# Performance work log

Hardware: AMD Instinct MI355X
Metric: run time of the kernel (lower is better)

Reference implementation:

```python
import jax, jax.numpy as jnp
import numpy as np

DIM, H, KV, HD = 2048, 32, 8, 64
NREP = H // KV
EPS = 1e-6
NEG = -1e30


def _rope(x, cos, sin):
    # x: [B,S,h,HD], cos/sin: [S,HD//2]
    xr, xi = x[..., 0::2], x[..., 1::2]
    c = cos[None, :, None, :]
    s = sin[None, :, None, :]
    out = jnp.stack([xr * c - xi * s, xr * s + xi * c], axis=-1)
    return out.reshape(x.shape)


def _rmsnorm(x, w):
    xf = x.astype(jnp.float32)
    inv = jax.lax.rsqrt(jnp.mean(xf * xf, axis=-1, keepdims=True) + EPS)
    return (xf * inv * w).astype(x.dtype)


def setup_inputs() -> dict:
    key = jax.random.key(0)
    ks = jax.random.split(key, 9)
    B, S = 1, 2048
    x = jax.random.normal(ks[0], (B, S, DIM), jnp.float32)
    cos = jax.random.uniform(ks[1], (S, HD // 2), jnp.float32)
    sin = jax.random.uniform(ks[2], (S, HD // 2), jnp.float32)
    sc = 1.0 / np.sqrt(DIM)
    wq = jax.random.normal(ks[3], (DIM, DIM), jnp.float32) * sc
    wk = jax.random.normal(ks[4], (KV * HD, DIM), jnp.float32) * sc
    wv = jax.random.normal(ks[5], (KV * HD, DIM), jnp.float32) * sc
    wo = jax.random.normal(ks[6], (DIM, DIM), jnp.float32) * sc
    wg = jax.random.normal(ks[7], (DIM, DIM), jnp.float32) * sc
    qn = jnp.ones((HD,), jnp.float32)
    kn = jnp.ones((HD,), jnp.float32)
    return {"x": x, "cos": cos, "sin": sin, "wq": wq, "wk": wk, "wv": wv,
            "wo": wo, "wg": wg, "qn": qn, "kn": kn}


def reference(x, cos, sin, wq, wk, wv, wo, wg, qn, kn):
    B, S, _ = x.shape
    q = (x @ wq.T).reshape(B, S, H, HD)
    k = (x @ wk.T).reshape(B, S, KV, HD)
    v = (x @ wv.T).reshape(B, S, KV, HD)
    q = _rope(q, cos, sin)
    k = _rope(k, cos, sin)
    q = _rmsnorm(q, qn)
    k = _rmsnorm(k, kn)
    # GQA without materializing repeat_kv: head h = g*NREP + r uses kv head g
    qg = q.reshape(B, S, KV, NREP, HD)
    scale = 1.0 / np.sqrt(HD)
    scores = jnp.einsum('bqgrd,bkgd->bgrqk', qg, k) * scale  # [B,KV,NREP,S,S]
    causal = jnp.tril(jnp.ones((S, S), bool))
    scores = jnp.where(causal, scores, NEG)
    attn = jax.nn.softmax(scores, axis=-1)
    o = jnp.einsum('bgrqk,bkgd->bqgrd', attn, v).reshape(B, S, DIM)
    o = o * jax.nn.sigmoid(x @ wg.T)
    return o @ wo.T
```

## Files before the change

### kernel.cpp

```cpp
#include <hip/hip_runtime.h>
#include <stdint.h>

typedef unsigned short u16;
typedef __bf16 bf16x8 __attribute__((ext_vector_type(8)));
typedef float f32x4 __attribute__((ext_vector_type(4)));

__device__ __forceinline__ float bf2f(u16 u) {
  union { unsigned int i; float f; } v; v.i = ((unsigned int)u) << 16; return v.f;
}
__device__ __forceinline__ u16 f2bf(float f) {
  union { float f; unsigned int i; } v; v.f = f;
  unsigned int r = v.i + 0x7fffu + ((v.i >> 16) & 1u);
  return (u16)(r >> 16);
}
__device__ __forceinline__ u16 f2bf_trunc(float f) {
  union { float f; unsigned int i; } v; v.f = f;
  return (u16)(v.i >> 16);
}
__device__ __forceinline__ void ld16(const void* g, void* l) {
  __builtin_amdgcn_global_load_lds(
      (const __attribute__((address_space(1))) unsigned int*)g,
      (__attribute__((address_space(3))) unsigned int*)l, 16, 0, 0);
}

__global__ __launch_bounds__(256) void k_cast(
    const float* __restrict__ s0, u16* __restrict__ d0,
    const float* __restrict__ s1, u16* __restrict__ d1,
    const float* __restrict__ s2, u16* __restrict__ d2,
    const float* __restrict__ s3, u16* __restrict__ d3,
    const float* __restrict__ s4, u16* __restrict__ d4,
    const float* __restrict__ s5, u16* __restrict__ d5)
{
  int b = blockIdx.x;
  const float* s; u16* d;
  if (b < 4096)       { s = s0; d = d0; }
  else if (b < 8192)  { s = s1; d = d1; b -= 4096; }
  else if (b < 9216)  { s = s2; d = d2; b -= 8192; }
  else if (b < 10240) { s = s3; d = d3; b -= 9216; }
  else if (b < 14336) { s = s4; d = d4; b -= 10240; }
  else                { s = s5; d = d5; b -= 14336; }
  const int i = (b * 256 + threadIdx.x) * 4;
  const float4 v = *(const float4*)(s + i);
  ushort4 o;
  o.x = f2bf(v.x); o.y = f2bf(v.y); o.z = f2bf(v.z); o.w = f2bf(v.w);
  *(ushort4*)(d + i) = o;
}

template <typename OT>
__device__ __forceinline__ void gemm_body(
    const u16* __restrict__ A, int lda,
    const u16* __restrict__ B, int ldb,
    OT* __restrict__ C, int ldc, int K,
    u16* As, u16* Bs)
{
  const int tid = threadIdx.x;
  const int wave = tid >> 6, lane = tid & 63;
  const int wrow = (wave >> 1) * 64, wcol = (wave & 1) * 64;
  const int fr = lane & 15, kg = lane >> 4;
  const int srl = lane >> 3;
  const int scg = (lane & 7) ^ srl;

  f32x4 acc[4][4];
  const f32x4 z = {0.f, 0.f, 0.f, 0.f};
  for (int i = 0; i < 4; i++) for (int j = 0; j < 4; j++) acc[i][j] = z;

  const u16* Ag = A + (size_t)(wave * 8 + srl) * lda + scg * 8;
  const u16* Bg = B + (size_t)(wave * 8 + srl) * ldb + scg * 8;
  u16* Asw = As + wave * 8 * 64;
  u16* Bsw = Bs + wave * 8 * 64;
  const int sxr = fr & 7;

  for (int k0 = 0; k0 < K; k0 += 64) {
    for (int i = 0; i < 4; i++) {
      ld16(Ag + k0 + (size_t)(i * 32) * lda, Asw + i * 32 * 64);
      ld16(Bg + k0 + (size_t)(i * 32) * ldb, Bsw + i * 32 * 64);
    }
    __syncthreads();
    bf16x8 af[4][2], bfr[4][2];
    for (int i = 0; i < 4; i++)
      for (int h = 0; h < 2; h++) {
        af[i][h]  = *(const bf16x8*)&As[(wrow + i * 16 + fr) * 64 + (((h * 4 + kg) ^ sxr)) * 8];
        bfr[i][h] = *(const bf16x8*)&Bs[(wcol + i * 16 + fr) * 64 + (((h * 4 + kg) ^ sxr)) * 8];
      }
    for (int h = 0; h < 2; h++)
      for (int mi = 0; mi < 4; mi++)
        for (int ni = 0; ni < 4; ni++)
          acc[mi][ni] = __builtin_amdgcn_mfma_f32_16x16x32_bf16(af[mi][h], bfr[ni][h], acc[mi][ni], 0, 0, 0);
    __syncthreads();
  }
  const int er = kg * 4, ec = fr;
  for (int mi = 0; mi < 4; mi++)
    for (int ni = 0; ni < 4; ni++)
      for (int r = 0; r < 4; r++) {
        const float v = acc[mi][ni][r];
        OT* p = C + (size_t)(wrow + mi * 16 + er + r) * ldc + wcol + ni * 16 + ec;
        if constexpr (sizeof(OT) == 2) *p = (OT)f2bf(v); else *p = (OT)v;
      }
}

__global__ __launch_bounds__(256) void k_gemm_qkvg(
    const u16* __restrict__ x, const u16* __restrict__ wq, const u16* __restrict__ wk,
    const u16* __restrict__ wv, const u16* __restrict__ wg, u16* __restrict__ out)
{
  __shared__ __align__(16) u16 As[128 * 64];
  __shared__ __align__(16) u16 Bs[128 * 64];
  const int m0 = blockIdx.x * 128;
  const int c0 = blockIdx.y * 128;
  const u16* B; int br;
  if (c0 < 2048)      { B = wq; br = c0; }
  else if (c0 < 2560) { B = wk; br = c0 - 2048; }
  else if (c0 < 3072) { B = wv; br = c0 - 2560; }
  else                { B = wg; br = c0 - 3072; }
  gemm_body<u16>(x + (size_t)m0 * 2048, 2048, B + (size_t)br * 2048, 2048,
                 out + (size_t)m0 * 5120 + c0, 5120, 2048, As, Bs);
}

__global__ __launch_bounds__(256) void k_gemm_out(
    const u16* __restrict__ a, const u16* __restrict__ wo, float* __restrict__ out)
{
  __shared__ __align__(16) u16 As[128 * 64];
  __shared__ __align__(16) u16 Bs[128 * 64];
  const int m0 = blockIdx.x * 128;
  const int c0 = blockIdx.y * 128;
  gemm_body<float>(a + (size_t)m0 * 2048, 2048, wo + (size_t)c0 * 2048, 2048,
                   out + (size_t)m0 * 2048 + c0, 2048, 2048, As, Bs);
}

__global__ __launch_bounds__(256) void k_prep(
    u16* __restrict__ qkvg, const float* __restrict__ cosp, const float* __restrict__ sinp,
    const float* __restrict__ qn, const float* __restrict__ kn, u16* __restrict__ vt)
{
  __shared__ u16 Ls[64 * 72];
  if (blockIdx.x < 10240) {
    const int wid = (blockIdx.x * 256 + threadIdx.x) >> 6;
    const int lane = threadIdx.x & 63;
    const int s = wid / 20, hp = wid - s * 20;
    const int h = hp * 2 + (lane >> 5);
    const int j = lane & 31;
    u16* base; const float* wn;
    if (h < 32) { base = qkvg + (size_t)s * 5120 + h * 64;                wn = qn; }
    else        { base = qkvg + (size_t)s * 5120 + 2048 + (h - 32) * 64; wn = kn; }
    const unsigned int u = *(const unsigned int*)(base + 2 * j);
    const float xr = bf2f((u16)(u & 0xffffu)), xi = bf2f((u16)(u >> 16));
    const float c = cosp[s * 32 + j], sn = sinp[s * 32 + j];
    const float o0 = xr * c - xi * sn;
    const float o1 = xr * sn + xi * c;
    float ss = o0 * o0 + o1 * o1;
    for (int m = 1; m <= 16; m <<= 1) ss += __shfl_xor(ss, m, 64);
    const float inv = rsqrtf(ss * (1.0f / 64.0f) + 1e-6f);
    const u16 r0 = f2bf(o0 * inv * wn[2 * j]);
    const u16 r1 = f2bf(o1 * inv * wn[2 * j + 1]);
    *(unsigned int*)(base + 2 * j) = (unsigned int)r0 | ((unsigned int)r1 << 16);
  } else {
    const int bb = blockIdx.x - 10240;
    const int s0 = (bb & 31) * 64, g0 = (bb >> 5) * 64;
    const int tid = threadIdx.x;
    const int lr = tid >> 4, lc = (tid & 15) * 4;
    for (int p = 0; p < 4; p++) {
      const int r = p * 16 + lr;
      *(ushort4*)&Ls[r * 72 + lc] = *(const ushort4*)&qkvg[(size_t)(s0 + r) * 5120 + 2560 + g0 + lc];
    }
    __syncthreads();
    for (int p = 0; p < 4; p++) {
      const int r = p * 16 + lr;
      ushort4 o;
      o.x = Ls[(lc + 0) * 72 + r];
      o.y = Ls[(lc + 1) * 72 + r];
      o.z = Ls[(lc + 2) * 72 + r];
      o.w = Ls[(lc + 3) * 72 + r];
      *(ushort4*)&vt[(size_t)(g0 + r) * 2048 + s0 + lc] = o;
    }
  }
}

__global__ __launch_bounds__(256, 3) void k_attn_part(
    const u16* __restrict__ qkvg, const u16* __restrict__ vt,
    u16* __restrict__ part, float* __restrict__ ml)
{
  __shared__ __align__(16) u16 Ks[128 * 64];
  __shared__ __align__(16) u16 Vs[64 * 128];
  __shared__ __align__(16) u16 Ps[64 * 132];
  const int c = blockIdx.x, h = blockIdx.y, g = h >> 2;
  int qt, ci;
  if (c < 4)       { qt = c;                  ci = 0; }
  else if (c < 12) { qt = 4 + ((c - 4) >> 1);   ci = (c - 4) & 1; }
  else if (c < 24) { qt = 8 + (c - 12) / 3;     ci = (c - 12) % 3; }
  else             { qt = 12 + ((c - 24) >> 2); ci = (c - 24) & 3; }
  const int kb0 = ci * 512;
  const int kend = min(kb0 + 512, (qt + 1) * 128);
  const int q0 = qt * 128;
  const int tid = threadIdx.x, wave = tid >> 6, lane = tid & 63;
  const int fr = lane & 15, kg = lane >> 4, fq = kg * 8;
  const int sx = fr & 7;

  {
    const u16* Qg = qkvg + (size_t)(q0 + wave * 32 + (lane >> 3)) * 5120 + h * 64 + (lane & 7) * 8;
    for (int i = 0; i < 4; i++)
      ld16(Qg + (size_t)(i * 8) * 5120, Ks + (wave * 32 + i * 8) * 64);
  }
  __syncthreads();
  bf16x8 aq[2][2];
  for (int rb = 0; rb < 2; rb++) {
    aq[rb][0] = *(const bf16x8*)&Ks[(rb * 64 + wave * 16 + fr) * 64 + fq];
    aq[rb][1] = *(const bf16x8*)&Ks[(rb * 64 + wave * 16 + fr) * 64 + 32 + fq];
  }
  __syncthreads();

  f32x4 o[2][4];
  const f32x4 z = {0.f, 0.f, 0.f, 0.f};
  for (int rb = 0; rb < 2; rb++) for (int i = 0; i < 4; i++) o[rb][i] = z;
  float lsum[2][4] = {{0.f,0.f,0.f,0.f},{0.f,0.f,0.f,0.f}};

  const int krl = wave * 8 + (lane >> 3);
  const int kcg = (lane & 7) ^ (krl & 7);
  const int vrl = wave * 4 + kg;
  const int vcg = fr ^ (vrl & 7);
  const u16* Kg = qkvg + (size_t)(kb0 + krl) * 5120 + 2048 + g * 64 + kcg * 8;
  const u16* Vg = vt + (size_t)(g * 64 + vrl) * 2048 + kb0 + vcg * 8;

  for (int kb = kb0; kb < kend; kb += 128) {
    for (int i = 0; i < 4; i++)
      ld16(Kg + (size_t)(i * 32) * 5120, Ks + (i * 32 + wave * 8) * 64);
    for (int i = 0; i < 4; i++)
      ld16(Vg + (size_t)(i * 16) * 2048, Vs + (i * 16 + wave * 4) * 128);
    Kg += (size_t)128 * 5120;
    Vg += 128;
    __syncthreads();

    for (int rb = 0; rb < 2; rb++) {
      f32x4 sc[8];
      for (int i = 0; i < 8; i++) sc[i] = z;
      for (int ni = 0; ni < 8; ni++) {
        const bf16x8 bk0 = *(const bf16x8*)&Ks[(ni * 16 + fr) * 64 + (kg ^ sx) * 8];
        const bf16x8 bk1 = *(const bf16x8*)&Ks[(ni * 16 + fr) * 64 + ((kg + 4) ^ sx) * 8];
        sc[ni] = __builtin_amdgcn_mfma_f32_16x16x32_bf16(aq[rb][0], bk0, sc[ni], 0, 0, 0);
        sc[ni] = __builtin_amdgcn_mfma_f32_16x16x32_bf16(aq[rb][1], bk1, sc[ni], 0, 0, 0);
      }

      const int qrow = q0 + rb * 64 + wave * 16 + kg * 4;
      for (int r = 0; r < 4; r++) {
        float ls = 0.f;
        for (int ni = 0; ni < 8; ni++) {
          const int key = kb + ni * 16 + fr;
          float p = __expf(fmaf(sc[ni][r], 0.125f, -8.0f));
          p = (key <= qrow + r) ? p : 0.f;
          ls += p;
          Ps[(wave * 16 + kg * 4 + r) * 132 + ni * 16 + fr] = f2bf_trunc(p);
        }
        lsum[rb][r] += ls;
      }

      for (int k0 = 0; k0 < 128; k0 += 32) {
        const bf16x8 ap = *(const bf16x8*)&Ps[(wave * 16 + fr) * 132 + k0 + fq];
        for (int ni = 0; ni < 4; ni++) {
          const bf16x8 bv = *(const bf16x8*)&Vs[(ni * 16 + fr) * 128 + (((k0 >> 3) + kg) ^ sx) * 8];
          o[rb][ni] = __builtin_amdgcn_mfma_f32_16x16x32_bf16(ap, bv, o[rb][ni], 0, 0, 0);
        }
      }
    }
    __syncthreads();
  }

  const int pbase = (h * 40 + c) * 8192;
  for (int rb = 0; rb < 2; rb++)
    for (int r = 0; r < 4; r++) {
      float L = lsum[rb][r];
      for (int m = 1; m <= 8; m <<= 1) L += __shfl_xor(L, m, 64);
      const int rl = rb * 64 + wave * 16 + kg * 4 + r;
      for (int ni = 0; ni < 4; ni++)
        part[pbase + rl * 64 + ni * 16 + fr] = f2bf(o[rb][ni][r]);
      if (fr == 0) ml[(h * 40 + c) * 128 + rl] = L;
    }
}

__global__ __launch_bounds__(256) void k_attn_comb(
    const u16* __restrict__ part, const float* __restrict__ ml,
    const u16* __restrict__ qkvg, u16* __restrict__ aout)
{
  const int qt = blockIdx.x, h = blockIdx.y;
  const int w = threadIdx.x >> 6, lane = threadIdx.x & 63;
  int cb, nch;
  if (qt < 4)       { cb = qt;                nch = 1; }
  else if (qt < 8)  { cb = 4 + 2 * (qt - 4);   nch = 2; }
  else if (qt < 12) { cb = 12 + 3 * (qt - 8);  nch = 3; }
  else              { cb = 24 + 4 * (qt - 12); nch = 4; }
  for (int r = 0; r < 32; r++) {
    const int rl = w * 32 + r;
    const int row = qt * 128 + rl;
    float L = 0.f, o = 0.f;
    for (int cc = 0; cc < nch; cc++) {
      L += ml[(h * 40 + cb + cc) * 128 + rl];
      o += bf2f(part[(h * 40 + cb + cc) * 8192 + rl * 64 + lane]);
    }
    const float gv = bf2f(qkvg[(size_t)row * 5120 + 3072 + h * 64 + lane]);
    const float sig = 1.0f / (1.0f + __expf(-gv));
    aout[(size_t)row * 2048 + h * 64 + lane] = f2bf(o / L * sig);
  }
}

extern "C" void kernel_launch(void* const* d_in, const int* in_sizes, int n_in,
                              void* d_out, int out_size, void* d_ws, size_t ws_size,
                              hipStream_t stream)
{
  const float* x  = (const float*)d_in[0];
  const float* cs = (const float*)d_in[1];
  const float* sn = (const float*)d_in[2];
  const float* wq = (const float*)d_in[3];
  const float* wk = (const float*)d_in[4];
  const float* wv = (const float*)d_in[5];
  const float* wo = (const float*)d_in[6];
  const float* wg = (const float*)d_in[7];
  const float* qn = (const float*)d_in[8];
  const float* kn = (const float*)d_in[9];
  float* out = (float*)d_out;

  u16* xb   = (u16*)d_ws;
  u16* wqb  = xb  + (size_t)4194304;
  u16* wkb  = wqb + (size_t)4194304;
  u16* wvb  = wkb + (size_t)1048576;
  u16* wgb  = wvb + (size_t)1048576;
  u16* wob  = wgb + (size_t)4194304;
  u16* qkvg = wob + (size_t)4194304;
  u16* vt   = qkvg + (size_t)2048 * 5120;
  u16* aws  = vt   + (size_t)512 * 2048;

  u16*   part = xb;
  float* ml   = (float*)(xb + (size_t)32 * 40 * 8192);

  k_cast<<<dim3(18432), 256, 0, stream>>>(x, xb, wq, wqb, wk, wkb, wv, wvb, wo, wob, wg, wgb);
  k_gemm_qkvg<<<dim3(16, 40), 256, 0, stream>>>(xb, wqb, wkb, wvb, wgb, qkvg);
  k_prep<<<dim3(10240 + 256), 256, 0, stream>>>(qkvg, cs, sn, qn, kn, vt);
  k_attn_part<<<dim3(40, 32), 256, 0, stream>>>(qkvg, vt, part, ml);
  k_attn_comb<<<dim3(16, 32), 256, 0, stream>>>(part, ml, qkvg, aws);
  k_gemm_out<<<dim3(16, 16), 256, 0, stream>>>(aws, wob, out);
}
```

Measured before the change: 316.1 us.

## Fuse RoPE, RMSNorm and V transpose into QKVG GEMM epilogue

Removes the separate prep kernel by applying RoPE and per-head RMSNorm to Q/K tiles, and transposing V into vt, directly inside the QKVG GEMM epilogue. The adjacent real/imag pair is fetched with a lane shuffle and the head sum of squares is reduced over 16 lanes. This saves one launch and a full read/modify/write pass over Q, K and V in global memory. In exchange the epilogue becomes heavier and branches per column tile, and the shared gemm body is inlined by hand into both kernels.

```diff
diff --git a/kernel.cpp b/kernel.cpp
--- a/kernel.cpp
+++ b/kernel.cpp
@@ -46,61 +46,12 @@
   *(ushort4*)(d + i) = o;
 }
 
-template <typename OT>
-__device__ __forceinline__ void gemm_body(
-    const u16* __restrict__ A, int lda,
-    const u16* __restrict__ B, int ldb,
-    OT* __restrict__ C, int ldc, int K,
-    u16* As, u16* Bs)
-{
-  const int tid = threadIdx.x;
-  const int wave = tid >> 6, lane = tid & 63;
-  const int wrow = (wave >> 1) * 64, wcol = (wave & 1) * 64;
-  const int fr = lane & 15, kg = lane >> 4;
-  const int srl = lane >> 3;
-  const int scg = (lane & 7) ^ srl;
-
-  f32x4 acc[4][4];
-  const f32x4 z = {0.f, 0.f, 0.f, 0.f};
-  for (int i = 0; i < 4; i++) for (int j = 0; j < 4; j++) acc[i][j] = z;
-
-  const u16* Ag = A + (size_t)(wave * 8 + srl) * lda + scg * 8;
-  const u16* Bg = B + (size_t)(wave * 8 + srl) * ldb + scg * 8;
-  u16* Asw = As + wave * 8 * 64;
-  u16* Bsw = Bs + wave * 8 * 64;
-  const int sxr = fr & 7;
-
-  for (int k0 = 0; k0 < K; k0 += 64) {
-    for (int i = 0; i < 4; i++) {
-      ld16(Ag + k0 + (size_t)(i * 32) * lda, Asw + i * 32 * 64);
-      ld16(Bg + k0 + (size_t)(i * 32) * ldb, Bsw + i * 32 * 64);
-    }
-    __syncthreads();
-    bf16x8 af[4][2], bfr[4][2];
-    for (int i = 0; i < 4; i++)
-      for (int h = 0; h < 2; h++) {
-        af[i][h]  = *(const bf16x8*)&As[(wrow + i * 16 + fr) * 64 + (((h * 4 + kg) ^ sxr)) * 8];
-        bfr[i][h] = *(const bf16x8*)&Bs[(wcol + i * 16 + fr) * 64 + (((h * 4 + kg) ^ sxr)) * 8];
-      }
-    for (int h = 0; h < 2; h++)
-      for (int mi = 0; mi < 4; mi++)
-        for (int ni = 0; ni < 4; ni++)
-          acc[mi][ni] = __builtin_amdgcn_mfma_f32_16x16x32_bf16(af[mi][h], bfr[ni][h], acc[mi][ni], 0, 0, 0);
-    __syncthreads();
-  }
-  const int er = kg * 4, ec = fr;
-  for (int mi = 0; mi < 4; mi++)
-    for (int ni = 0; ni < 4; ni++)
-      for (int r = 0; r < 4; r++) {
-        const float v = acc[mi][ni][r];
-        OT* p = C + (size_t)(wrow + mi * 16 + er + r) * ldc + wcol + ni * 16 + ec;
-        if constexpr (sizeof(OT) == 2) *p = (OT)f2bf(v); else *p = (OT)v;
-      }
-}
-
 __global__ __launch_bounds__(256) void k_gemm_qkvg(
     const u16* __restrict__ x, const u16* __restrict__ wq, const u16* __restrict__ wk,
-    const u16* __restrict__ wv, const u16* __restrict__ wg, u16* __restrict__ out)
+    const u16* __restrict__ wv, const u16* __restrict__ wg,
+    u16* __restrict__ qkvg, u16* __restrict__ vt,
+    const float* __restrict__ cosp, const float* __restrict__ sinp,
+    const float* __restrict__ qn, const float* __restrict__ kn)
 {
   __shared__ __align__(16) u16 As[128 * 64];
   __shared__ __align__(16) u16 Bs[128 * 64];
@@ -111,8 +62,83 @@
   else if (c0 < 2560) { B = wk; br = c0 - 2048; }
   else if (c0 < 3072) { B = wv; br = c0 - 2560; }
   else                { B = wg; br = c0 - 3072; }
-  gemm_body<u16>(x + (size_t)m0 * 2048, 2048, B + (size_t)br * 2048, 2048,
-                 out + (size_t)m0 * 5120 + c0, 5120, 2048, As, Bs);
+
+  const int tid = threadIdx.x;
+  const int wave = tid >> 6, lane = tid & 63;
+  const int wrow = (wave >> 1) * 64, wcol = (wave & 1) * 64;
+  const int fr = lane & 15, kg = lane >> 4;
+  const int srl = lane >> 3;
+  const int scg = (lane & 7) ^ srl;
+
+  f32x4 acc[4][4];
+  const f32x4 z = {0.f, 0.f, 0.f, 0.f};
+  for (int i = 0; i < 4; i++) for (int j = 0; j < 4; j++) acc[i][j] = z;
+
+  const u16* Ag = x + (size_t)(m0 + wave * 8 + srl) * 2048 + scg * 8;
+  const u16* Bg = B + (size_t)(br + wave * 8 + srl) * 2048 + scg * 8;
+  u16* Asw = As + wave * 8 * 64;
+  u16* Bsw = Bs + wave * 8 * 64;
+  const int sxr = fr & 7;
+
+  for (int k0 = 0; k0 < 2048; k0 += 64) {
+    for (int i = 0; i < 4; i++) {
+      ld16(Ag + k0 + (size_t)(i * 32) * 2048, Asw + i * 32 * 64);
+      ld16(Bg + k0 + (size_t)(i * 32) * 2048, Bsw + i * 32 * 64);
+    }
+    __syncthreads();
+    bf16x8 af[4][2], bfr[4][2];
+    for (int i = 0; i < 4; i++)
+      for (int h = 0; h < 2; h++) {
+        af[i][h]  = *(const bf16x8*)&As[(wrow + i * 16 + fr) * 64 + (((h * 4 + kg) ^ sxr)) * 8];
+        bfr[i][h] = *(const bf16x8*)&Bs[(wcol + i * 16 + fr) * 64 + (((h * 4 + kg) ^ sxr)) * 8];
+      }
+    for (int h = 0; h < 2; h++)
+      for (int mi = 0; mi < 4; mi++)
+        for (int ni = 0; ni < 4; ni++)
+          acc[mi][ni] = __builtin_amdgcn_mfma_f32_16x16x32_bf16(af[mi][h], bfr[ni][h], acc[mi][ni], 0, 0, 0);
+    __syncthreads();
+  }
+
+  const int er = kg * 4, ec = fr;
+  if (c0 >= 2560 && c0 < 3072) {
+    for (int mi = 0; mi < 4; mi++)
+      for (int ni = 0; ni < 4; ni++) {
+        ushort4 st;
+        st.x = f2bf(acc[mi][ni][0]); st.y = f2bf(acc[mi][ni][1]);
+        st.z = f2bf(acc[mi][ni][2]); st.w = f2bf(acc[mi][ni][3]);
+        const int gd = (c0 - 2560) + wcol + ni * 16 + ec;
+        const int s  = m0 + wrow + mi * 16 + er;
+        *(ushort4*)&vt[(size_t)gd * 2048 + s] = st;
+      }
+  } else if (c0 < 2560) {
+    const float* wnp = (c0 < 2048) ? qn : kn;
+    float wv4[4];
+    for (int ni = 0; ni < 4; ni++) wv4[ni] = wnp[ni * 16 + ec];
+    const int odd = ec & 1;
+    for (int mi = 0; mi < 4; mi++)
+      for (int r = 0; r < 4; r++) {
+        const int srow = m0 + wrow + mi * 16 + er + r;
+        float ov[4], ss = 0.f;
+        for (int ni = 0; ni < 4; ni++) {
+          const float v = acc[mi][ni][r];
+          const float p = __shfl_xor(v, 1, 64);
+          const int j = ni * 8 + (ec >> 1);
+          const float cc = cosp[srow * 32 + j], sv = sinp[srow * 32 + j];
+          const float o = odd ? (p * sv + v * cc) : (v * cc - p * sv);
+          ov[ni] = o; ss += o * o;
+        }
+        for (int m = 1; m <= 8; m <<= 1) ss += __shfl_xor(ss, m, 64);
+        const float inv = rsqrtf(ss * (1.0f / 64.0f) + 1e-6f);
+        for (int ni = 0; ni < 4; ni++)
+          qkvg[(size_t)srow * 5120 + c0 + wcol + ni * 16 + ec] = f2bf(ov[ni] * inv * wv4[ni]);
+      }
+  } else {
+    for (int mi = 0; mi < 4; mi++)
+      for (int ni = 0; ni < 4; ni++)
+        for (int r = 0; r < 4; r++)
+          qkvg[(size_t)(m0 + wrow + mi * 16 + er + r) * 5120 + c0 + wcol + ni * 16 + ec] =
+              f2bf(acc[mi][ni][r]);
+  }
 }
 
 __global__ __launch_bounds__(256) void k_gemm_out(
@@ -122,55 +148,47 @@
   __shared__ __align__(16) u16 Bs[128 * 64];
   const int m0 = blockIdx.x * 128;
   const int c0 = blockIdx.y * 128;
-  gemm_body<float>(a + (size_t)m0 * 2048, 2048, wo + (size_t)c0 * 2048, 2048,
-                   out + (size_t)m0 * 2048 + c0, 2048, 2048, As, Bs);
-}
-
-__global__ __launch_bounds__(256) void k_prep(
-    u16* __restrict__ qkvg, const float* __restrict__ cosp, const float* __restrict__ sinp,
-    const float* __restrict__ qn, const float* __restrict__ kn, u16* __restrict__ vt)
-{
-  __shared__ u16 Ls[64 * 72];
-  if (blockIdx.x < 10240) {
-    const int wid = (blockIdx.x * 256 + threadIdx.x) >> 6;
-    const int lane = threadIdx.x & 63;
-    const int s = wid / 20, hp = wid - s * 20;
-    const int h = hp * 2 + (lane >> 5);
-    const int j = lane & 31;
-    u16* base; const float* wn;
-    if (h < 32) { base = qkvg + (size_t)s * 5120 + h * 64;                wn = qn; }
-    else        { base = qkvg + (size_t)s * 5120 + 2048 + (h - 32) * 64; wn = kn; }
-    const unsigned int u = *(const unsigned int*)(base + 2 * j);
-    const float xr = bf2f((u16)(u & 0xffffu)), xi = bf2f((u16)(u >> 16));
-    const float c = cosp[s * 32 + j], sn = sinp[s * 32 + j];
-    const float o0 = xr * c - xi * sn;
-    const float o1 = xr * sn + xi * c;
-    float ss = o0 * o0 + o1 * o1;
-    for (int m = 1; m <= 16; m <<= 1) ss += __shfl_xor(ss, m, 64);
-    const float inv = rsqrtf(ss * (1.0f / 64.0f) + 1e-6f);
-    const u16 r0 = f2bf(o0 * inv * wn[2 * j]);
-    const u16 r1 = f2bf(o1 * inv * wn[2 * j + 1]);
-    *(unsigned int*)(base + 2 * j) = (unsigned int)r0 | ((unsigned int)r1 << 16);
-  } else {
-    const int bb = blockIdx.x - 10240;
-    const int s0 = (bb & 31) * 64, g0 = (bb >> 5) * 64;
-    const int tid = threadIdx.x;
-    const int lr = tid >> 4, lc = (tid & 15) * 4;
-    for (int p = 0; p < 4; p++) {
-      const int r = p * 16 + lr;
-      *(ushort4*)&Ls[r * 72 + lc] = *(const ushort4*)&qkvg[(size_t)(s0 + r) * 5120 + 2560 + g0 + lc];
-    }
-    __syncthreads();
-    for (int p = 0; p < 4; p++) {
-      const int r = p * 16 + lr;
-      ushort4 o;
-      o.x = Ls[(lc + 0) * 72 + r];
-      o.y = Ls[(lc + 1) * 72 + r];
-      o.z = Ls[(lc + 2) * 72 + r];
-      o.w = Ls[(lc + 3) * 72 + r];
-      *(ushort4*)&vt[(size_t)(g0 + r) * 2048 + s0 + lc] = o;
-    }
-  }
+  const int tid = threadIdx.x;
+  const int wave = tid >> 6, lane = tid & 63;
+  const int wrow = (wave >> 1) * 64, wcol = (wave & 1) * 64;
+  const int fr = lane & 15, kg = lane >> 4;
+  const int srl = lane >> 3;
+  const int scg = (lane & 7) ^ srl;
+
+  f32x4 acc[4][4];
+  const f32x4 z = {0.f, 0.f, 0.f, 0.f};
+  for (int i = 0; i < 4; i++) for (int j = 0; j < 4; j++) acc[i][j] = z;
+
+  const u16* Ag = a  + (size_t)(m0 + wave * 8 + srl) * 2048 + scg * 8;
+  const u16* Bg = wo + (size_t)(c0 + wave * 8 + srl) * 2048 + scg * 8;
+  u16* Asw = As + wave * 8 * 64;
+  u16* Bsw = Bs + wave * 8 * 64;
+  const int sxr = fr & 7;
+
+  for (int k0 = 0; k0 < 2048; k0 += 64) {
+    for (int i = 0; i < 4; i++) {
+      ld16(Ag + k0 + (size_t)(i * 32) * 2048, Asw + i * 32 * 64);
+      ld16(Bg + k0 + (size_t)(i * 32) * 2048, Bsw + i * 32 * 64);
+    }
+    __syncthreads();
+    bf16x8 af[4][2], bfr[4][2];
+    for (int i = 0; i < 4; i++)
+      for (int h = 0; h < 2; h++) {
+        af[i][h]  = *(const bf16x8*)&As[(wrow + i * 16 + fr) * 64 + (((h * 4 + kg) ^ sxr)) * 8];
+        bfr[i][h] = *(const bf16x8*)&Bs[(wcol + i * 16 + fr) * 64 + (((h * 4 + kg) ^ sxr)) * 8];
+      }
+    for (int h = 0; h < 2; h++)
+      for (int mi = 0; mi < 4; mi++)
+        for (int ni = 0; ni < 4; ni++)
+          acc[mi][ni] = __builtin_amdgcn_mfma_f32_16x16x32_bf16(af[mi][h], bfr[ni][h], acc[mi][ni], 0, 0, 0);
+    __syncthreads();
+  }
+  const int er = kg * 4, ec = fr;
+  for (int mi = 0; mi < 4; mi++)
+    for (int ni = 0; ni < 4; ni++)
+      for (int r = 0; r < 4; r++)
+        out[(size_t)(m0 + wrow + mi * 16 + er + r) * 2048 + c0 + wcol + ni * 16 + ec] =
+            acc[mi][ni][r];
 }
 
 __global__ __launch_bounds__(256, 3) void k_attn_part(
@@ -328,8 +346,7 @@
   float* ml   = (float*)(xb + (size_t)32 * 40 * 8192);
 
   k_cast<<<dim3(18432), 256, 0, stream>>>(x, xb, wq, wqb, wk, wkb, wv, wvb, wo, wob, wg, wgb);
-  k_gemm_qkvg<<<dim3(16, 40), 256, 0, stream>>>(xb, wqb, wkb, wvb, wgb, qkvg);
-  k_prep<<<dim3(10240 + 256), 256, 0, stream>>>(qkvg, cs, sn, qn, kn, vt);
+  k_gemm_qkvg<<<dim3(16, 40), 256, 0, stream>>>(xb, wqb, wkb, wvb, wgb, qkvg, vt, cs, sn, qn, kn);
   k_attn_part<<<dim3(40, 32), 256, 0, stream>>>(qkvg, vt, part, ml);
   k_attn_comb<<<dim3(16, 32), 256, 0, stream>>>(part, ml, qkvg, aws);
   k_gemm_out<<<dim3(16, 16), 256, 0, stream>>>(aws, wob, out);
```

Result: slower. 327.1 us (+3.5%).
